# Kernel optimization log

Measured on AMD Instinct MI355X. Metric: run time of the kernel, lower is better.

## Reference

```python
import jax, jax.numpy as jnp
import numpy as np

N_NODES = 100000
N_EDGES = 1600000
D_IN = 64
D_OUT = 64
ROW_WINDOW = 16  # TCGNN row-window size (metadata only)


def setup_inputs() -> dict:
    key = jax.random.key(0)
    ks = jax.random.split(key, 7)
    X = jax.random.normal(ks[0], (N_NODES, D_IN), dtype=jnp.float32)
    weights = jax.random.normal(ks[1], (D_IN, D_OUT), dtype=jnp.float32)
    # CSR row pointers: sorted offsets into the edge list, endpoints pinned.
    rp = jnp.sort(jax.random.randint(ks[2], (N_NODES + 1,), 0, N_EDGES, dtype=jnp.int32))
    row_pointers = rp.at[0].set(0).at[-1].set(N_EDGES)
    column_index = jax.random.randint(ks[3], (N_EDGES,), 0, N_NODES, dtype=jnp.int32)
    # TCGNN tiling metadata (does not affect the math; kept for signature fidelity)
    blockPartition = jax.random.randint(ks[4], (N_NODES // ROW_WINDOW,), 0, 8, dtype=jnp.int32)
    edgeToColumn = jax.random.randint(ks[5], (N_EDGES,), 0, N_NODES, dtype=jnp.int32)
    edgeToRow = jax.random.randint(ks[6], (N_EDGES,), 0, N_NODES, dtype=jnp.int32)
    return {
        "X": X,
        "weights": weights,
        "row_pointers": row_pointers,
        "column_index": column_index,
        "blockPartition": blockPartition,
        "edgeToColumn": edgeToColumn,
        "edgeToRow": edgeToRow,
    }


def reference(X, weights, row_pointers, column_index, blockPartition, edgeToColumn, edgeToRow):
    # TCGNN.forward == unweighted CSR SpMM: X_prime[i] = sum_{j in N(i)} X[j]
    n_edges = column_index.shape[0]
    # Map each edge position to its CSR row id.
    row_ids = jnp.searchsorted(row_pointers, jnp.arange(n_edges, dtype=row_pointers.dtype), side="right") - 1
    gathered = X[column_index]  # [n_edges, d_in] irregular gather
    X_prime = jax.ops.segment_sum(gathered, row_ids, num_segments=X.shape[0])  # [n_nodes, d_in]
    return X_prime @ weights  # dense GEMM [n_nodes, d_out]
```

## Files before the change

kernel.cpp:

```cpp
#include <hip/hip_runtime.h>
#include <cstdint>
#include <cstddef>

#define D 64

typedef float    f32x4 __attribute__((ext_vector_type(4)));
typedef short    s16x8 __attribute__((ext_vector_type(8)));
typedef uint32_t u32x4 __attribute__((ext_vector_type(4)));

__device__ __forceinline__ uint32_t rne_bf16(float f) {
    uint32_t x = __float_as_uint(f);
    return (x + 0x7fffu + ((x >> 16) & 1u)) >> 16;
}
__device__ __forceinline__ float bf16lo(uint32_t u) { return __uint_as_float(u << 16); }
__device__ __forceinline__ float bf16hi(uint32_t u) { return __uint_as_float(u & 0xffff0000u); }

__global__ __launch_bounds__(256) void cast_kernel(
    const float* __restrict__ X, uint32_t* __restrict__ Xh, long n4)
{
    long i = (long)blockIdx.x * blockDim.x + threadIdx.x;
    const long stride = (long)gridDim.x * blockDim.x;
    for (; i < n4; i += stride) {
        f32x4 v = __builtin_nontemporal_load((const f32x4*)X + i);
        uint2 o;
        o.x = rne_bf16(v.x) | (rne_bf16(v.y) << 16);
        o.y = rne_bf16(v.z) | (rne_bf16(v.w) << 16);
        ((uint2*)Xh)[i] = o;
    }
}

__global__ __launch_bounds__(256) void gather3_kernel(
    const uint32_t* __restrict__ Xh, const int* __restrict__ rp,
    const int* __restrict__ ci, uint32_t* __restrict__ Agg, int n_nodes)
{
    const int lane = threadIdx.x & 63;
    const int o = lane >> 3;
    const int p = lane & 7;
    const int row = (int)((blockIdx.x * blockDim.x + threadIdx.x) >> 6);
    if (row >= n_nodes) return;

    const int e0 = rp[row];
    const int e1 = rp[row + 1];

    float a[8] = {0,0,0,0,0,0,0,0};
    float b[8] = {0,0,0,0,0,0,0,0};

    int e = e0;
    for (; e + 32 <= e1; e += 32) {
        const int i0 = ci[e      + o];
        const int i1 = ci[e +  8 + o];
        const int i2 = ci[e + 16 + o];
        const int i3 = ci[e + 24 + o];
        const u32x4 u0 = *(const u32x4*)(Xh + (size_t)i0 * 32 + p * 4);
        const u32x4 u1 = *(const u32x4*)(Xh + (size_t)i1 * 32 + p * 4);
        const u32x4 u2 = *(const u32x4*)(Xh + (size_t)i2 * 32 + p * 4);
        const u32x4 u3 = *(const u32x4*)(Xh + (size_t)i3 * 32 + p * 4);
#pragma unroll
        for (int k = 0; k < 4; ++k) {
            a[2*k] += bf16lo(u0[k]); a[2*k+1] += bf16hi(u0[k]);
            b[2*k] += bf16lo(u1[k]); b[2*k+1] += bf16hi(u1[k]);
            a[2*k] += bf16lo(u2[k]); a[2*k+1] += bf16hi(u2[k]);
            b[2*k] += bf16lo(u3[k]); b[2*k+1] += bf16hi(u3[k]);
        }
    }
    if (e + 16 <= e1) {
        const int i0 = ci[e     + o];
        const int i1 = ci[e + 8 + o];
        const u32x4 u0 = *(const u32x4*)(Xh + (size_t)i0 * 32 + p * 4);
        const u32x4 u1 = *(const u32x4*)(Xh + (size_t)i1 * 32 + p * 4);
#pragma unroll
        for (int k = 0; k < 4; ++k) {
            a[2*k] += bf16lo(u0[k]); a[2*k+1] += bf16hi(u0[k]);
            b[2*k] += bf16lo(u1[k]); b[2*k+1] += bf16hi(u1[k]);
        }
        e += 16;
    }
    if (e + 8 <= e1) {
        const int i0 = ci[e + o];
        const u32x4 u0 = *(const u32x4*)(Xh + (size_t)i0 * 32 + p * 4);
#pragma unroll
        for (int k = 0; k < 4; ++k) {
            a[2*k] += bf16lo(u0[k]); a[2*k+1] += bf16hi(u0[k]);
        }
        e += 8;
    }
    if (o < e1 - e) {
        const int i0 = ci[e + o];
        const u32x4 u0 = *(const u32x4*)(Xh + (size_t)i0 * 32 + p * 4);
#pragma unroll
        for (int k = 0; k < 4; ++k) {
            b[2*k] += bf16lo(u0[k]); b[2*k+1] += bf16hi(u0[k]);
        }
    }

#pragma unroll
    for (int j = 0; j < 8; ++j) {
        float v = a[j] + b[j];
        v += __shfl_xor(v, 8, 64);
        v += __shfl_xor(v, 16, 64);
        v += __shfl_xor(v, 32, 64);
        a[j] = v;
    }
    if (lane < 8) {
        u32x4 w;
#pragma unroll
        for (int k = 0; k < 4; ++k)
            w[k] = rne_bf16(a[2*k]) | (rne_bf16(a[2*k+1]) << 16);
        *(u32x4*)(Agg + (size_t)row * 32 + p * 4) = w;
    }
}

__global__ __launch_bounds__(256) void agg_gemm_kernel(
    const uint32_t* __restrict__ Agg, const float* __restrict__ W,
    float* __restrict__ out, int n_nodes)
{
    const int lane = threadIdx.x & 63;
    const int n = lane & 15;
    const int q = lane >> 4;

    s16x8 Bf[4][2];
#pragma unroll
    for (int c = 0; c < 4; ++c)
#pragma unroll
        for (int kb = 0; kb < 2; ++kb) {
            s16x8 bfr;
#pragma unroll
            for (int j = 0; j < 8; ++j) {
                const int k = kb * 32 + q * 8 + j;
                bfr[j] = (short)rne_bf16(W[k * D + c * 16 + n]);
            }
            Bf[c][kb] = bfr;
        }

    const int n_tiles = (n_nodes + 15) / 16;
    const int gwave = (int)((blockIdx.x * blockDim.x + threadIdx.x) >> 6);
    const int nwaves = (int)((gridDim.x * blockDim.x) >> 6);

    for (int t = gwave; t < n_tiles; t += nwaves) {
        const int m0 = t * 16;
        int arow = m0 + n;
        if (arow >= n_nodes) arow = n_nodes - 1;
        const s16x8 A0 = *(const s16x8*)(Agg + (size_t)arow * 32 + q * 4);
        const s16x8 A1 = *(const s16x8*)(Agg + (size_t)arow * 32 + 16 + q * 4);

        f32x4 acc[4];
#pragma unroll
        for (int c = 0; c < 4; ++c) {
            f32x4 z = {0.f, 0.f, 0.f, 0.f};
            z = __builtin_amdgcn_mfma_f32_16x16x32_bf16(A0, Bf[c][0], z, 0, 0, 0);
            z = __builtin_amdgcn_mfma_f32_16x16x32_bf16(A1, Bf[c][1], z, 0, 0, 0);
            acc[c] = z;
        }
#pragma unroll
        for (int r = 0; r < 4; ++r) {
            const int ro = m0 + q * 4 + r;
            if (ro < n_nodes) {
#pragma unroll
                for (int c = 0; c < 4; ++c)
                    out[(size_t)ro * D + c * 16 + n] = acc[c][r];
            }
        }
    }
}

__global__ __launch_bounds__(256) void fused_kernel(
    const float* __restrict__ X, const float* __restrict__ W,
    const int* __restrict__ rp, const int* __restrict__ ci,
    float* __restrict__ out, int n_nodes)
{
    __shared__ float Wl[D * D];
    for (int i = threadIdx.x; i < D * D; i += 256) Wl[i] = W[i];
    __syncthreads();

    const int lane = threadIdx.x & 63;
    const int gwave = (int)((blockIdx.x * blockDim.x + threadIdx.x) >> 6);
    const int nwaves = (int)((gridDim.x * blockDim.x) >> 6);

    for (int row = gwave; row < n_nodes; row += nwaves) {
        int e0 = rp[row];
        int e1 = rp[row + 1];
        float acc = 0.f;
        for (int e = e0; e < e1; ++e) acc += X[ci[e] * D + lane];
        float sum = 0.f;
#pragma unroll
        for (int d = 0; d < D; ++d) {
            float a = __shfl(acc, d, 64);
            sum += a * Wl[d * D + lane];
        }
        out[row * D + lane] = sum;
    }
}

extern "C" void kernel_launch(void* const* d_in, const int* in_sizes, int n_in,
                              void* d_out, int out_size, void* d_ws, size_t ws_size,
                              hipStream_t stream)
{
    const float* X  = (const float*)d_in[0];
    const float* W  = (const float*)d_in[1];
    const int*   rp = (const int*)d_in[2];
    const int*   ci = (const int*)d_in[3];
    float* out = (float*)d_out;

    const int n_nodes = in_sizes[2] - 1;
    const size_t row_bytes = 32 * sizeof(uint32_t);
    const size_t need = 2 * (size_t)n_nodes * row_bytes;

    if (ws_size >= need) {
        uint32_t* Xh  = (uint32_t*)d_ws;
        uint32_t* Agg = (uint32_t*)((char*)d_ws + (size_t)n_nodes * row_bytes);

        const long n4 = (long)n_nodes * (D / 4);
        int cast_blocks = (int)((n4 + 255) / 256);
        if (cast_blocks > 6400) cast_blocks = 6400;
        cast_kernel<<<cast_blocks, 256, 0, stream>>>(X, Xh, n4);

        const int gather_blocks = (n_nodes + 3) / 4;
        gather3_kernel<<<gather_blocks, 256, 0, stream>>>(Xh, rp, ci, Agg, n_nodes);

        const int n_tiles = (n_nodes + 15) / 16;
        const int gemm_blocks = (n_tiles + 3) / 4;
        agg_gemm_kernel<<<gemm_blocks, 256, 0, stream>>>(Agg, W, out, n_nodes);
    } else {
        fused_kernel<<<2048, 256, 0, stream>>>(X, W, rp, ci, out, n_nodes);
    }
}
```

Measured before the change: 146.3 us.

## Fuse sparse gather and bf16 MFMA GEMM into one kernel via LDS tile

The separate gather and GEMM kernels become one kernel. Each 256-thread block aggregates 16 rows, four per wave, into a shared-memory bf16 tile, then each wave runs MFMA for one 16-column slice of the output. This removes the Agg round-trip through global memory and one kernel launch, and output stores become nontemporal. In exchange, each wave now handles four rows serially with no overlap, adds a block barrier, and recomputes the W fragments in every block.

```diff
diff --git a/kernel.cpp b/kernel.cpp
--- a/kernel.cpp
+++ b/kernel.cpp
@@ -29,137 +29,123 @@
     }
 }
 
-__global__ __launch_bounds__(256) void gather3_kernel(
-    const uint32_t* __restrict__ Xh, const int* __restrict__ rp,
-    const int* __restrict__ ci, uint32_t* __restrict__ Agg, int n_nodes)
-{
-    const int lane = threadIdx.x & 63;
-    const int o = lane >> 3;
-    const int p = lane & 7;
-    const int row = (int)((blockIdx.x * blockDim.x + threadIdx.x) >> 6);
-    if (row >= n_nodes) return;
-
-    const int e0 = rp[row];
-    const int e1 = rp[row + 1];
-
-    float a[8] = {0,0,0,0,0,0,0,0};
-    float b[8] = {0,0,0,0,0,0,0,0};
-
-    int e = e0;
-    for (; e + 32 <= e1; e += 32) {
-        const int i0 = ci[e      + o];
-        const int i1 = ci[e +  8 + o];
-        const int i2 = ci[e + 16 + o];
-        const int i3 = ci[e + 24 + o];
-        const u32x4 u0 = *(const u32x4*)(Xh + (size_t)i0 * 32 + p * 4);
-        const u32x4 u1 = *(const u32x4*)(Xh + (size_t)i1 * 32 + p * 4);
-        const u32x4 u2 = *(const u32x4*)(Xh + (size_t)i2 * 32 + p * 4);
-        const u32x4 u3 = *(const u32x4*)(Xh + (size_t)i3 * 32 + p * 4);
-#pragma unroll
-        for (int k = 0; k < 4; ++k) {
-            a[2*k] += bf16lo(u0[k]); a[2*k+1] += bf16hi(u0[k]);
-            b[2*k] += bf16lo(u1[k]); b[2*k+1] += bf16hi(u1[k]);
-            a[2*k] += bf16lo(u2[k]); a[2*k+1] += bf16hi(u2[k]);
-            b[2*k] += bf16lo(u3[k]); b[2*k+1] += bf16hi(u3[k]);
-        }
-    }
-    if (e + 16 <= e1) {
-        const int i0 = ci[e     + o];
-        const int i1 = ci[e + 8 + o];
-        const u32x4 u0 = *(const u32x4*)(Xh + (size_t)i0 * 32 + p * 4);
-        const u32x4 u1 = *(const u32x4*)(Xh + (size_t)i1 * 32 + p * 4);
-#pragma unroll
-        for (int k = 0; k < 4; ++k) {
-            a[2*k] += bf16lo(u0[k]); a[2*k+1] += bf16hi(u0[k]);
-            b[2*k] += bf16lo(u1[k]); b[2*k+1] += bf16hi(u1[k]);
-        }
-        e += 16;
-    }
-    if (e + 8 <= e1) {
-        const int i0 = ci[e + o];
-        const u32x4 u0 = *(const u32x4*)(Xh + (size_t)i0 * 32 + p * 4);
-#pragma unroll
-        for (int k = 0; k < 4; ++k) {
-            a[2*k] += bf16lo(u0[k]); a[2*k+1] += bf16hi(u0[k]);
-        }
-        e += 8;
-    }
-    if (o < e1 - e) {
-        const int i0 = ci[e + o];
-        const u32x4 u0 = *(const u32x4*)(Xh + (size_t)i0 * 32 + p * 4);
-#pragma unroll
-        for (int k = 0; k < 4; ++k) {
-            b[2*k] += bf16lo(u0[k]); b[2*k+1] += bf16hi(u0[k]);
-        }
-    }
-
-#pragma unroll
-    for (int j = 0; j < 8; ++j) {
-        float v = a[j] + b[j];
-        v += __shfl_xor(v, 8, 64);
-        v += __shfl_xor(v, 16, 64);
-        v += __shfl_xor(v, 32, 64);
-        a[j] = v;
-    }
-    if (lane < 8) {
-        u32x4 w;
-#pragma unroll
-        for (int k = 0; k < 4; ++k)
-            w[k] = rne_bf16(a[2*k]) | (rne_bf16(a[2*k+1]) << 16);
-        *(u32x4*)(Agg + (size_t)row * 32 + p * 4) = w;
-    }
-}
-
-__global__ __launch_bounds__(256) void agg_gemm_kernel(
-    const uint32_t* __restrict__ Agg, const float* __restrict__ W,
+__global__ __launch_bounds__(256) void fused_gather_gemm_kernel(
+    const uint32_t* __restrict__ Xh, const float* __restrict__ W,
+    const int* __restrict__ rp, const int* __restrict__ ci,
     float* __restrict__ out, int n_nodes)
 {
-    const int lane = threadIdx.x & 63;
-    const int n = lane & 15;
-    const int q = lane >> 4;
-
-    s16x8 Bf[4][2];
-#pragma unroll
-    for (int c = 0; c < 4; ++c)
-#pragma unroll
-        for (int kb = 0; kb < 2; ++kb) {
-            s16x8 bfr;
-#pragma unroll
-            for (int j = 0; j < 8; ++j) {
-                const int k = kb * 32 + q * 8 + j;
-                bfr[j] = (short)rne_bf16(W[k * D + c * 16 + n]);
-            }
-            Bf[c][kb] = bfr;
-        }
-
-    const int n_tiles = (n_nodes + 15) / 16;
-    const int gwave = (int)((blockIdx.x * blockDim.x + threadIdx.x) >> 6);
-    const int nwaves = (int)((gridDim.x * blockDim.x) >> 6);
-
-    for (int t = gwave; t < n_tiles; t += nwaves) {
-        const int m0 = t * 16;
-        int arow = m0 + n;
-        if (arow >= n_nodes) arow = n_nodes - 1;
-        const s16x8 A0 = *(const s16x8*)(Agg + (size_t)arow * 32 + q * 4);
-        const s16x8 A1 = *(const s16x8*)(Agg + (size_t)arow * 32 + 16 + q * 4);
-
-        f32x4 acc[4];
-#pragma unroll
-        for (int c = 0; c < 4; ++c) {
-            f32x4 z = {0.f, 0.f, 0.f, 0.f};
-            z = __builtin_amdgcn_mfma_f32_16x16x32_bf16(A0, Bf[c][0], z, 0, 0, 0);
-            z = __builtin_amdgcn_mfma_f32_16x16x32_bf16(A1, Bf[c][1], z, 0, 0, 0);
-            acc[c] = z;
-        }
-#pragma unroll
-        for (int r = 0; r < 4; ++r) {
-            const int ro = m0 + q * 4 + r;
-            if (ro < n_nodes) {
-#pragma unroll
-                for (int c = 0; c < 4; ++c)
-                    out[(size_t)ro * D + c * 16 + n] = acc[c][r];
-            }
-        }
+    __shared__ __align__(16) uint32_t tileA[16 * 32];
+
+    const int tid  = threadIdx.x;
+    const int lane = tid & 63;
+    const int wv   = tid >> 6;
+    const int o    = lane >> 3;
+    const int p    = lane & 7;
+    const int n    = lane & 15;
+    const int q    = lane >> 4;
+
+    s16x8 Bf[2];
+#pragma unroll
+    for (int kb = 0; kb < 2; ++kb) {
+        s16x8 bfr;
+#pragma unroll
+        for (int j = 0; j < 8; ++j) {
+            const int k = kb * 32 + q * 8 + j;
+            bfr[j] = (short)rne_bf16(W[k * D + wv * 16 + n]);
+        }
+        Bf[kb] = bfr;
+    }
+
+    const int m0 = blockIdx.x * 16;
+
+#pragma unroll 1
+    for (int rr = 0; rr < 4; ++rr) {
+        const int row = m0 + wv * 4 + rr;
+
+        float a[8] = {0,0,0,0,0,0,0,0};
+        float b[8] = {0,0,0,0,0,0,0,0};
+
+        if (row < n_nodes) {
+            const int e0 = rp[row];
+            const int e1 = rp[row + 1];
+            int e = e0;
+            for (; e + 32 <= e1; e += 32) {
+                const int i0 = ci[e      + o];
+                const int i1 = ci[e +  8 + o];
+                const int i2 = ci[e + 16 + o];
+                const int i3 = ci[e + 24 + o];
+                const u32x4 u0 = *(const u32x4*)(Xh + (size_t)i0 * 32 + p * 4);
+                const u32x4 u1 = *(const u32x4*)(Xh + (size_t)i1 * 32 + p * 4);
+                const u32x4 u2 = *(const u32x4*)(Xh + (size_t)i2 * 32 + p * 4);
+                const u32x4 u3 = *(const u32x4*)(Xh + (size_t)i3 * 32 + p * 4);
+#pragma unroll
+                for (int k = 0; k < 4; ++k) {
+                    a[2*k] += bf16lo(u0[k]); a[2*k+1] += bf16hi(u0[k]);
+                    b[2*k] += bf16lo(u1[k]); b[2*k+1] += bf16hi(u1[k]);
+                    a[2*k] += bf16lo(u2[k]); a[2*k+1] += bf16hi(u2[k]);
+                    b[2*k] += bf16lo(u3[k]); b[2*k+1] += bf16hi(u3[k]);
+                }
+            }
+            if (e + 16 <= e1) {
+                const int i0 = ci[e     + o];
+                const int i1 = ci[e + 8 + o];
+                const u32x4 u0 = *(const u32x4*)(Xh + (size_t)i0 * 32 + p * 4);
+                const u32x4 u1 = *(const u32x4*)(Xh + (size_t)i1 * 32 + p * 4);
+#pragma unroll
+                for (int k = 0; k < 4; ++k) {
+                    a[2*k] += bf16lo(u0[k]); a[2*k+1] += bf16hi(u0[k]);
+                    b[2*k] += bf16lo(u1[k]); b[2*k+1] += bf16hi(u1[k]);
+                }
+                e += 16;
+            }
+            if (e + 8 <= e1) {
+                const int i0 = ci[e + o];
+                const u32x4 u0 = *(const u32x4*)(Xh + (size_t)i0 * 32 + p * 4);
+#pragma unroll
+                for (int k = 0; k < 4; ++k) {
+                    a[2*k] += bf16lo(u0[k]); a[2*k+1] += bf16hi(u0[k]);
+                }
+                e += 8;
+            }
+            if (o < e1 - e) {
+                const int i0 = ci[e + o];
+                const u32x4 u0 = *(const u32x4*)(Xh + (size_t)i0 * 32 + p * 4);
+#pragma unroll
+                for (int k = 0; k < 4; ++k) {
+                    b[2*k] += bf16lo(u0[k]); b[2*k+1] += bf16hi(u0[k]);
+                }
+            }
+        }
+
+#pragma unroll
+        for (int j = 0; j < 8; ++j) {
+            float v = a[j] + b[j];
+            v += __shfl_xor(v, 8, 64);
+            v += __shfl_xor(v, 16, 64);
+            v += __shfl_xor(v, 32, 64);
+            a[j] = v;
+        }
+        if (lane < 8) {
+            u32x4 wrow;
+#pragma unroll
+            for (int k = 0; k < 4; ++k)
+                wrow[k] = rne_bf16(a[2*k]) | (rne_bf16(a[2*k+1]) << 16);
+            *(u32x4*)(tileA + (wv * 4 + rr) * 32 + p * 4) = wrow;
+        }
+    }
+
+    __syncthreads();
+
+    const s16x8 A0 = *(const s16x8*)(tileA + n * 32 + q * 4);
+    const s16x8 A1 = *(const s16x8*)(tileA + n * 32 + 16 + q * 4);
+    f32x4 z = {0.f, 0.f, 0.f, 0.f};
+    z = __builtin_amdgcn_mfma_f32_16x16x32_bf16(A0, Bf[0], z, 0, 0, 0);
+    z = __builtin_amdgcn_mfma_f32_16x16x32_bf16(A1, Bf[1], z, 0, 0, 0);
+#pragma unroll
+    for (int r = 0; r < 4; ++r) {
+        const int ro = m0 + q * 4 + r;
+        if (ro < n_nodes)
+            __builtin_nontemporal_store(z[r], out + (size_t)ro * D + wv * 16 + n);
     }
 }
 
@@ -202,24 +188,18 @@
     float* out = (float*)d_out;
 
     const int n_nodes = in_sizes[2] - 1;
-    const size_t row_bytes = 32 * sizeof(uint32_t);
-    const size_t need = 2 * (size_t)n_nodes * row_bytes;
+    const size_t need = (size_t)n_nodes * 32 * sizeof(uint32_t);
 
     if (ws_size >= need) {
-        uint32_t* Xh  = (uint32_t*)d_ws;
-        uint32_t* Agg = (uint32_t*)((char*)d_ws + (size_t)n_nodes * row_bytes);
+        uint32_t* Xh = (uint32_t*)d_ws;
 
         const long n4 = (long)n_nodes * (D / 4);
         int cast_blocks = (int)((n4 + 255) / 256);
         if (cast_blocks > 6400) cast_blocks = 6400;
         cast_kernel<<<cast_blocks, 256, 0, stream>>>(X, Xh, n4);
 
-        const int gather_blocks = (n_nodes + 3) / 4;
-        gather3_kernel<<<gather_blocks, 256, 0, stream>>>(Xh, rp, ci, Agg, n_nodes);
-
-        const int n_tiles = (n_nodes + 15) / 16;
-        const int gemm_blocks = (n_tiles + 3) / 4;
-        agg_gemm_kernel<<<gemm_blocks, 256, 0, stream>>>(Agg, W, out, n_nodes);
+        const int tiles = (n_nodes + 15) / 16;
+        fused_gather_gemm_kernel<<<tiles, 256, 0, stream>>>(Xh, W, rp, ci, out, n_nodes);
     } else {
         fused_kernel<<<2048, 256, 0, stream>>>(X, W, rp, ci, out, n_nodes);
     }
```

Result: no change. 148.3 us (+1.4%).
